# Optimization experiments

Measured on AMD Instinct MI355X. Metric: run time of the kernel, lower is better.

The kernel has to match this reference:

```python
import jax, jax.numpy as jnp
import numpy as np

N, K, C_S, C_Z, C_G, N_RBF = 1024, 16, 256, 128, 16, 64
EPS = 1e-8


def _ln(x, g, b, eps=1e-5):
    m = x.mean(-1, keepdims=True)
    v = jnp.mean((x - m) ** 2, -1, keepdims=True)
    return (x - m) * jax.lax.rsqrt(v + eps) * g + b


def _rbf(D, D_count=N_RBF, D_min=0.0, D_max=20.0):
    mu = jnp.linspace(D_min, D_max, D_count, dtype=D.dtype)
    sigma = (D_max - D_min) / D_count
    return jnp.exp(-(((D[..., None] - mu) / sigma) ** 2))


def setup_inputs() -> dict:
    key = jax.random.key(0)
    ks = jax.random.split(key, 20)
    node_features = jax.random.normal(ks[0], (N, C_S), jnp.float32)
    trans = jax.random.normal(ks[1], (N, 3), jnp.float32) * 5.0  # CA translations, Angstrom-ish
    edge_features = jax.random.normal(ks[2], (N * K, C_Z), jnp.float32)
    # sparse graph laid out as K neighbors per node: dst = node i repeated K times
    src = jax.random.randint(ks[3], (N * K,), 0, N)
    dst = jnp.repeat(jnp.arange(N), K)
    edge_index = jnp.stack([src, dst]).astype(jnp.int64)
    batch = jnp.zeros((N,), jnp.int64)
    res_mask = jnp.ones((N,), bool)
    w = lambda k, i, o: jax.random.normal(k, (i, o), jnp.float32) * 0.02
    return {
        "node_features": node_features, "trans": trans, "edge_features": edge_features,
        "ln_g": jnp.ones((C_Z,), jnp.float32), "ln_b": jnp.zeros((C_Z,), jnp.float32),
        "Wl": w(ks[4], C_S, C_G), "bl": jnp.zeros((C_G,), jnp.float32),
        "Wr": w(ks[5], C_S, C_G), "br": jnp.zeros((C_G,), jnp.float32),
        "Wep": w(ks[6], C_Z, C_Z), "bep": jnp.zeros((C_Z,), jnp.float32),
        "Weg": w(ks[7], C_Z, C_Z), "beg": jnp.zeros((C_Z,), jnp.float32),
        "Wdg": w(ks[8], C_G * C_G, C_Z), "bdg": jnp.zeros((C_Z,), jnp.float32),
        "Wdp": w(ks[9], N_RBF, C_Z), "bdp": jnp.zeros((C_Z,), jnp.float32),
        "lno_g": jnp.ones((C_Z,), jnp.float32), "lno_b": jnp.zeros((C_Z,), jnp.float32),
        "Wout": w(ks[10], C_Z, C_Z), "bout": jnp.zeros((C_Z,), jnp.float32),
        "Wog": w(ks[11], C_Z, C_Z), "bog": jnp.zeros((C_Z,), jnp.float32),
        "edge_index": edge_index, "batch": batch, "res_mask": res_mask,
    }


def reference(node_features, trans, edge_features, ln_g, ln_b, Wl, bl, Wr, br,
              Wep, bep, Weg, beg, Wdg, bdg, Wdp, bdp, lno_g, lno_b, Wout, bout,
              Wog, bog, edge_index, batch, res_mask):
    n = node_features.shape[0]
    src = edge_index[0].reshape(n, K)              # neighbor indices per node [N,K]
    # sparse -> kNN: edges are grouped K per destination node
    knn_feats = edge_features.reshape(n, K, C_Z)
    knn_mask = res_mask[src] & res_mask[:, None]   # [N,K]
    z = _ln(knn_feats, ln_g, ln_b)
    # outer-product node gating
    nl = node_features @ Wl + bl                   # [N,c_g]
    nr = node_features @ Wr + br
    a = nl[src]                                    # [N,K,c_g]
    b = nr[src]
    edge3 = a[:, :, None, :, None] * b[:, None, :, None, :]   # [N,K,K,c_g,c_g]
    gate3 = edge3.reshape(n, K, K, C_G * C_G) @ Wdg + bdg     # [N,K,K,c_z]
    # RBF distance features among the K neighbors of each node
    t = trans[src]                                 # [N,K,3]
    d = jnp.linalg.norm(t[:, :, None, :] - t[:, None, :, :] + EPS, axis=-1)  # [N,K,K]
    df = _rbf(d) @ Wdp + bdp                       # [N,K,K,c_z]
    m2 = (knn_mask[:, :, None] & knn_mask[:, None, :]).astype(df.dtype)
    e3 = jax.nn.sigmoid(gate3) * df * m2[..., None]
    # gated edge projection
    e2 = jax.nn.sigmoid(z @ Weg + beg) * (z @ Wep + bep)      # [N,K,c_z]
    # triangle matmul: per channel c, [K,K] @ [K]
    upd = jnp.einsum('njkc,nkc->njc', e3, e2)                 # [N,K,c_z]
    upd = _ln(upd, lno_g, lno_b) @ Wout + bout
    upd = upd * jax.nn.sigmoid(z @ Wog + bog)
    # kNN -> sparse scatter back (masked)
    out = (upd * knn_mask[..., None].astype(upd.dtype)).reshape(n * K, C_Z)
    return out
```

## Files before the change

kernel.cpp:

```cpp
#include <hip/hip_runtime.h>
#include <hip/hip_bf16.h>
#include <math.h>

#define KNN  16
#define CZ   128
#define CG   16
#define CS   256
#define NRBF 64
#define NN   1024

typedef __attribute__((ext_vector_type(8))) _Float16 half8;
typedef __attribute__((ext_vector_type(4))) _Float16 half4;
typedef __attribute__((ext_vector_type(2))) _Float16 half2v;
typedef __attribute__((ext_vector_type(4))) float f4_t;

#define MFMA16x32(A, B, C) __builtin_amdgcn_mfma_f32_16x16x32_f16((A), (B), (C), 0, 0, 0)
#define MFMA16x16(A, B, C) __builtin_amdgcn_mfma_f32_16x16x16f16((A), (B), (C), 0, 0, 0)

union U8 { half2v h[4]; half8 v; };
union U4 { half2v h[2]; half4 v; };

__device__ __forceinline__ half2v pk2(float x, float y) {
    auto t = __builtin_amdgcn_cvt_pkrtz(x, y);
    half2v r;
    __builtin_memcpy(&r, &t, 4);
    return r;
}
__device__ __forceinline__ float sig_(float x) {
    return __builtin_amdgcn_rcpf(1.0f + __expf(-x));
}

__global__ __launch_bounds__(256) void prep_kernel(
    const float* __restrict__ Wdp, const float* __restrict__ Wdg,
    const float* __restrict__ Wout, const float* __restrict__ Wep,
    const float* __restrict__ Weg, const float* __restrict__ Wog,
    _Float16* __restrict__ pk,
    const float* __restrict__ nf,
    const float* __restrict__ Wl, const float* __restrict__ bl,
    const float* __restrict__ Wr, const float* __restrict__ br,
    float* __restrict__ nlo, float* __restrict__ nro) {
    int b = blockIdx.x, tid = threadIdx.x;
    if (b < 416) {
        int gid = b * 256 + tid;
        float val;
        if (gid >= 8192 && gid < 40960) {
            int o = gid - 8192;
            int i = o & 3, l = (o >> 2) & 63, ct = (o >> 8) & 7, q = o >> 11;
            int row = (4 * (l >> 4) + i) * 16 + q;
            int col = ct * 16 + (l & 15);
            val = Wdg[row * CZ + col];
        } else {
            const float* srcw;
            int o;
            if (gid < 8192)        { srcw = Wdp;  o = gid; }
            else if (gid < 57344)  { srcw = Wout; o = gid - 40960; }
            else if (gid < 73728)  { srcw = Wep;  o = gid - 57344; }
            else if (gid < 90112)  { srcw = Weg;  o = gid - 73728; }
            else                   { srcw = Wog;  o = gid - 90112; }
            int t = o & 7, l = (o >> 3) & 63, ct = (o >> 9) & 7, s = o >> 12;
            int row = s * 32 + (l >> 4) * 8 + t;
            int col = ct * 16 + (l & 15);
            val = srcw[row * CZ + col];
        }
        pk[gid] = (_Float16)val;
    } else {
        int grp = tid >> 6, lane = tid & 63;
        int n = (b - 416) * 4 + grp;
        int p = lane & 15, seg = lane >> 4;
        float accl = (seg == 0) ? bl[p] : 0.0f;
        float accr = (seg == 0) ? br[p] : 0.0f;
        const float* rw = nf + n * CS + seg * 64;
        for (int i = 0; i < 64; ++i) {
            float v = rw[i];
            int s = seg * 64 + i;
            accl += v * Wl[s * CG + p];
            accr += v * Wr[s * CG + p];
        }
        accl += __shfl_xor(accl, 16); accl += __shfl_xor(accl, 32);
        accr += __shfl_xor(accr, 16); accr += __shfl_xor(accr, 32);
        if (lane < 16) { nlo[n * CG + lane] = accl; nro[n * CG + lane] = accr; }
    }
}

__global__ __launch_bounds__(256) void main_kernel(
    const float* __restrict__ trans, const float* __restrict__ ef,
    const float* __restrict__ lng, const float* __restrict__ lnb,
    const float* __restrict__ nl, const float* __restrict__ nr,
    const float* __restrict__ bep, const float* __restrict__ beg,
    const float* __restrict__ bog,
    const _Float16* __restrict__ Wepp, const _Float16* __restrict__ Wegp,
    const _Float16* __restrict__ Wogp,
    const _Float16* __restrict__ Wdg2, const float* __restrict__ bdg,
    const _Float16* __restrict__ Wdpp, const float* __restrict__ bdp,
    const float* __restrict__ lnog, const float* __restrict__ lnob,
    const _Float16* __restrict__ Woutp, const float* __restrict__ bout,
    const int* __restrict__ src, const int* __restrict__ resmask,
    float* __restrict__ out) {
    __shared__ _Float16 s_z[16 * 136];
    __shared__ float s_t[16 * 4];
    __shared__ float s_km[16];
    __shared__ int   s_src[16];
    __shared__ float s_a[16 * 16];
    __shared__ float s_b[16 * 20];
    __shared__ _Float16 s_T[4][8192];
    __shared__ _Float16 s_upd[16 * 136];

    int n = blockIdx.x, tid = threadIdx.x;
    if (tid < 16) {
        int sv = src[n * KNN + tid];
        s_src[tid] = sv;
        s_km[tid] = (resmask[sv] != 0 && resmask[n] != 0) ? 1.0f : 0.0f;
        s_t[tid * 4 + 0] = trans[sv * 3 + 0];
        s_t[tid * 4 + 1] = trans[sv * 3 + 1];
        s_t[tid * 4 + 2] = trans[sv * 3 + 2];
    }
    __syncthreads();
    {
        int j = tid >> 4, p = tid & 15;
        int sv = s_src[j];
        s_a[j * 16 + p] = nl[sv * CG + p];
        s_b[j * 20 + p] = nr[sv * CG + p];
    }
    {
        int r = tid >> 4, seg = tid & 15;
        const float* row = ef + ((size_t)n * KNN + r) * CZ + seg * 8;
        f4_t x0 = *(const f4_t*)row;
        f4_t x1 = *(const f4_t*)(row + 4);
        float s = x0.x + x0.y + x0.z + x0.w + x1.x + x1.y + x1.z + x1.w;
        float q = x0.x * x0.x + x0.y * x0.y + x0.z * x0.z + x0.w * x0.w
                + x1.x * x1.x + x1.y * x1.y + x1.z * x1.z + x1.w * x1.w;
        #pragma unroll
        for (int m = 1; m < 16; m <<= 1) { s += __shfl_xor(s, m); q += __shfl_xor(q, m); }
        float mean = s * (1.0f / CZ);
        float var  = q * (1.0f / CZ) - mean * mean;
        float rs   = __builtin_amdgcn_rsqf(var + 1e-5f);
        int col = seg * 8;
        f4_t g0 = *(const f4_t*)(lng + col), g1 = *(const f4_t*)(lng + col + 4);
        f4_t b0 = *(const f4_t*)(lnb + col), b1 = *(const f4_t*)(lnb + col + 4);
        U8 zu;
        zu.h[0] = pk2((x0.x - mean) * rs * g0.x + b0.x, (x0.y - mean) * rs * g0.y + b0.y);
        zu.h[1] = pk2((x0.z - mean) * rs * g0.z + b0.z, (x0.w - mean) * rs * g0.w + b0.w);
        zu.h[2] = pk2((x1.x - mean) * rs * g1.x + b1.x, (x1.y - mean) * rs * g1.y + b1.y);
        zu.h[3] = pk2((x1.z - mean) * rs * g1.z + b1.z, (x1.w - mean) * rs * g1.w + b1.w);
        *(half8*)&s_z[r * 136 + col] = zu.v;
    }
    __syncthreads();

    int wv = tid >> 6, lane = tid & 63, l15 = lane & 15, quad = lane >> 4;

    half8 Az[4];
    #pragma unroll
    for (int st = 0; st < 4; ++st)
        Az[st] = *(const half8*)&s_z[l15 * 136 + st * 32 + quad * 8];
    f4_t e2f[2], ggf[2];
    #pragma unroll
    for (int cc = 0; cc < 2; ++cc) {
        int ct = wv * 2 + cc;
        int c = ct * 16 + l15;
        float vep = bep[c], veg = beg[c], vog = bog[c];
        f4_t aep = {vep, vep, vep, vep};
        f4_t aeg = {veg, veg, veg, veg};
        f4_t aog = {vog, vog, vog, vog};
        #pragma unroll
        for (int st = 0; st < 4; ++st) {
            int off = ((st * 8 + ct) * 64 + lane) * 8;
            half8 wep_ = *(const half8*)(Wepp + off);
            half8 weg_ = *(const half8*)(Wegp + off);
            half8 wog_ = *(const half8*)(Wogp + off);
            aep = MFMA16x32(Az[st], wep_, aep);
            aeg = MFMA16x32(Az[st], weg_, aeg);
            aog = MFMA16x32(Az[st], wog_, aog);
        }
        #pragma unroll
        for (int rr = 0; rr < 4; ++rr) {
            e2f[cc][rr] = sig_(aeg[rr]) * aep[rr] * s_km[quad * 4 + rr];
            ggf[cc][rr] = sig_(aog[rr]);
        }
    }

    half8 Bdp[2][2];
    #pragma unroll
    for (int st = 0; st < 2; ++st)
        #pragma unroll
        for (int cc = 0; cc < 2; ++cc)
            Bdp[st][cc] = *(const half8*)(Wdpp + ((st * 8 + wv * 2 + cc) * 64 + lane) * 8);

    half4 Aa, Ab;
    {
        f4_t av = *(const f4_t*)&s_a[l15 * 16 + 4 * quad];
        U4 u; u.h[0] = pk2(av.x, av.y); u.h[1] = pk2(av.z, av.w);
        Aa = u.v;
        f4_t bv = *(const f4_t*)&s_b[l15 * 20 + 4 * quad];
        U4 w; w.h[0] = pk2(bv.x, bv.y); w.h[1] = pk2(bv.z, bv.w);
        Ab = w.v;
    }
    _Float16* Tw = s_T[wv];
    #pragma unroll
    for (int ctl = 0; ctl < 2; ++ctl) {
        int ct = wv * 2 + ctl;
        #pragma unroll
        for (int q0 = 0; q0 < 16; q0 += 4) {
            f4_t tq[4];
            #pragma unroll
            for (int qq = 0; qq < 4; ++qq) {
                half4 Bw = *(const half4*)(Wdg2 + (((q0 + qq) * 8 + ct) * 64 + lane) * 4);
                f4_t z = {0.f, 0.f, 0.f, 0.f};
                tq[qq] = MFMA16x16(Aa, Bw, z);
            }
            #pragma unroll
            for (int rr = 0; rr < 4; ++rr) {
                U4 u;
                u.h[0] = pk2(tq[0][rr], tq[1][rr]);
                u.h[1] = pk2(tq[2][rr], tq[3][rr]);
                *(half4*)&Tw[(((4 * quad + rr) * 2 + ctl) * 16 + l15) * 16 + q0] = u.v;
            }
        }
    }

    float bdgv[2], bdpv[2];
    #pragma unroll
    for (int cc = 0; cc < 2; ++cc) {
        int c = (wv * 2 + cc) * 16 + l15;
        bdgv[cc] = bdg[c];
        bdpv[cc] = bdp[c];
    }
    float tkx = s_t[l15 * 4 + 0], tky = s_t[l15 * 4 + 1], tkz = s_t[l15 * 4 + 2];
    const float MUS = 20.0f / 63.0f;
    const float ISG = 1.0f / 0.3125f;
    float rIS[2];
    #pragma unroll
    for (int st = 0; st < 2; ++st)
        rIS[st] = (float)(st * 32 + quad * 8) * (MUS * ISG);

    for (int j = 0; j < 16; ++j) {
        float dx = s_t[j * 4 + 0] - tkx + 1e-8f;
        float dy = s_t[j * 4 + 1] - tky + 1e-8f;
        float dz = s_t[j * 4 + 2] - tkz + 1e-8f;
        float dI = sqrtf(dx * dx + dy * dy + dz * dz) * ISG;

        half8 ar[2];
        #pragma unroll
        for (int st = 0; st < 2; ++st) {
            U8 cv;
            float base0 = dI - rIS[st];
            #pragma unroll
            for (int tt = 0; tt < 4; ++tt) {
                float u0 = base0 - (float)(2 * tt) * (MUS * ISG);
                float u1 = u0 - (MUS * ISG);
                cv.h[tt] = pk2(__expf(-u0 * u0), __expf(-u1 * u1));
            }
            ar[st] = cv.v;
        }
        f4_t accd[2], accg[2];
        #pragma unroll
        for (int cc = 0; cc < 2; ++cc) {
            f4_t z = {bdpv[cc], bdpv[cc], bdpv[cc], bdpv[cc]};
            z = MFMA16x32(ar[0], Bdp[0][cc], z);
            z = MFMA16x32(ar[1], Bdp[1][cc], z);
            accd[cc] = z;
            half4 Bt = *(const half4*)&Tw[((j * 2 + cc) * 16 + l15) * 16 + 4 * quad];
            f4_t g = {bdgv[cc], bdgv[cc], bdgv[cc], bdgv[cc]};
            accg[cc] = MFMA16x16(Ab, Bt, g);
        }
        float kmj = s_km[j];
        #pragma unroll
        for (int cc = 0; cc < 2; ++cc) {
            float part = 0.f;
            #pragma unroll
            for (int rr = 0; rr < 4; ++rr)
                part += sig_(accg[cc][rr]) * accd[cc][rr] * e2f[cc][rr];
            part += __shfl_xor(part, 16);
            part += __shfl_xor(part, 32);
            if (lane < 16)
                s_upd[j * 136 + (wv * 2 + cc) * 16 + lane] = (_Float16)(part * kmj);
        }
    }
    __syncthreads();

    #pragma unroll
    for (int rr2 = 0; rr2 < 4; ++rr2) {
        int rj = wv * 4 + rr2;
        float x0 = (float)s_upd[rj * 136 + lane];
        float x1 = (float)s_upd[rj * 136 + 64 + lane];
        float sm = x0 + x1, sq = x0 * x0 + x1 * x1;
        #pragma unroll
        for (int m = 1; m < 64; m <<= 1) {
            sm += __shfl_xor(sm, m);
            sq += __shfl_xor(sq, m);
        }
        float mean = sm * (1.0f / CZ);
        float var  = sq * (1.0f / CZ) - mean * mean;
        float rsv  = __builtin_amdgcn_rsqf(var + 1e-5f);
        float h0 = (x0 - mean) * rsv * lnog[lane] + lnob[lane];
        float h1 = (x1 - mean) * rsv * lnog[64 + lane] + lnob[64 + lane];
        s_z[rj * 136 + lane]      = (_Float16)h0;
        s_z[rj * 136 + 64 + lane] = (_Float16)h1;
    }
    __syncthreads();

    half8 Aw[4];
    #pragma unroll
    for (int st = 0; st < 4; ++st)
        Aw[st] = *(const half8*)&s_z[l15 * 136 + st * 32 + quad * 8];
    #pragma unroll
    for (int cc = 0; cc < 2; ++cc) {
        int c = (wv * 2 + cc) * 16 + l15;
        float bo = bout[c];
        f4_t acc = {bo, bo, bo, bo};
        #pragma unroll
        for (int st = 0; st < 4; ++st) {
            half8 bw = *(const half8*)(Woutp + ((st * 8 + wv * 2 + cc) * 64 + lane) * 8);
            acc = MFMA16x32(Aw[st], bw, acc);
        }
        #pragma unroll
        for (int rr = 0; rr < 4; ++rr) {
            int row = quad * 4 + rr;
            size_t oi = (size_t)(n * KNN + row) * CZ + c;
            out[oi] = acc[rr] * ggf[cc][rr] * s_km[row];
        }
    }
}

extern "C" void kernel_launch(void* const* d_in, const int* in_sizes, int n_in,
                              void* d_out, int out_size, void* d_ws, size_t ws_size,
                              hipStream_t stream) {
    const float* node_features = (const float*)d_in[0];
    const float* trans         = (const float*)d_in[1];
    const float* edge_features = (const float*)d_in[2];
    const float* ln_g  = (const float*)d_in[3];
    const float* ln_b  = (const float*)d_in[4];
    const float* Wl    = (const float*)d_in[5];
    const float* bl    = (const float*)d_in[6];
    const float* Wr    = (const float*)d_in[7];
    const float* br    = (const float*)d_in[8];
    const float* Wep   = (const float*)d_in[9];
    const float* bep   = (const float*)d_in[10];
    const float* Weg   = (const float*)d_in[11];
    const float* beg   = (const float*)d_in[12];
    const float* Wdg   = (const float*)d_in[13];
    const float* bdg   = (const float*)d_in[14];
    const float* Wdp   = (const float*)d_in[15];
    const float* bdp   = (const float*)d_in[16];
    const float* lno_g = (const float*)d_in[17];
    const float* lno_b = (const float*)d_in[18];
    const float* Wout  = (const float*)d_in[19];
    const float* bout  = (const float*)d_in[20];
    const float* Wog   = (const float*)d_in[21];
    const float* bog   = (const float*)d_in[22];
    const int* edge_index = (const int*)d_in[23];
    const int* resmask    = (const int*)d_in[25];

    float* ws = (float*)d_ws;
    float* nl = ws;
    float* nr = nl + NN * CG;
    _Float16* pk = (_Float16*)(nr + NN * CG);
    _Float16* Wdpp  = pk;
    _Float16* Wdg2  = pk + 8192;
    _Float16* Woutp = pk + 40960;
    _Float16* Wepp  = pk + 57344;
    _Float16* Wegp  = pk + 73728;
    _Float16* Wogp  = pk + 90112;
    const int* src = edge_index;

    prep_kernel<<<672, 256, 0, stream>>>(
        Wdp, Wdg, Wout, Wep, Weg, Wog, pk,
        node_features, Wl, bl, Wr, br, nl, nr);
    main_kernel<<<NN, 256, 0, stream>>>(
        trans, edge_features, ln_g, ln_b, nl, nr,
        bep, beg, bog, Wepp, Wegp, Wogp,
        Wdg2, bdg, Wdpp, bdp, lno_g, lno_b,
        Woutp, bout, src, resmask, (float*)d_out);
}
```

Before: 163.2 us.

## Fuse weight prep and node projections into single kernel, halve triangle LDS buffer

Removes the separate prep kernel that repacked weights to fp16 and computed per-node left/right projections. The main kernel now reads fp32 weights directly with strided gathers and converts them into MFMA fragments in registers, and it computes the neighbor projections with MFMA per block. The Wdg-derived T buffer is built in two halves of eight neighbors each, shrinking LDS so more blocks can be resident. The cost is redundant uncoalesced weight loads and conversions in every block, plus recomputing T twice per half.

```diff
diff --git a/kernel.cpp b/kernel.cpp
--- a/kernel.cpp
+++ b/kernel.cpp
@@ -1,12 +1,10 @@
 #include <hip/hip_runtime.h>
-#include <hip/hip_bf16.h>
 #include <math.h>
 
 #define KNN  16
 #define CZ   128
 #define CG   16
 #define CS   256
-#define NRBF 64
 #define NN   1024
 
 typedef __attribute__((ext_vector_type(8))) _Float16 half8;
@@ -30,79 +28,53 @@
     return __builtin_amdgcn_rcpf(1.0f + __expf(-x));
 }
 
-__global__ __launch_bounds__(256) void prep_kernel(
-    const float* __restrict__ Wdp, const float* __restrict__ Wdg,
-    const float* __restrict__ Wout, const float* __restrict__ Wep,
-    const float* __restrict__ Weg, const float* __restrict__ Wog,
-    _Float16* __restrict__ pk,
-    const float* __restrict__ nf,
+__device__ __forceinline__ half8 gfrag(const float* __restrict__ W,
+                                       int st, int ct, int lane) {
+    int row = st * 32 + ((lane >> 4) << 3);
+    int col = ct * 16 + (lane & 15);
+    const float* p = W + row * CZ + col;
+    float v0 = p[0 * CZ], v1 = p[1 * CZ], v2 = p[2 * CZ], v3 = p[3 * CZ];
+    float v4 = p[4 * CZ], v5 = p[5 * CZ], v6 = p[6 * CZ], v7 = p[7 * CZ];
+    U8 u;
+    u.h[0] = pk2(v0, v1); u.h[1] = pk2(v2, v3);
+    u.h[2] = pk2(v4, v5); u.h[3] = pk2(v6, v7);
+    return u.v;
+}
+
+__device__ __forceinline__ half4 gfrag16(const float* __restrict__ Wdg,
+                                         int q, int ct, int lane) {
+    int quad = lane >> 4;
+    int col = ct * 16 + (lane & 15);
+    const float* p = Wdg + (4 * quad * 16 + q) * CZ + col;
+    float v0 = p[0 * 16 * CZ], v1 = p[1 * 16 * CZ];
+    float v2 = p[2 * 16 * CZ], v3 = p[3 * 16 * CZ];
+    U4 u;
+    u.h[0] = pk2(v0, v1); u.h[1] = pk2(v2, v3);
+    return u.v;
+}
+
+__global__ __launch_bounds__(256) void fused_kernel(
+    const float* __restrict__ nf, const float* __restrict__ trans,
+    const float* __restrict__ ef,
+    const float* __restrict__ lng, const float* __restrict__ lnb,
     const float* __restrict__ Wl, const float* __restrict__ bl,
     const float* __restrict__ Wr, const float* __restrict__ br,
-    float* __restrict__ nlo, float* __restrict__ nro) {
-    int b = blockIdx.x, tid = threadIdx.x;
-    if (b < 416) {
-        int gid = b * 256 + tid;
-        float val;
-        if (gid >= 8192 && gid < 40960) {
-            int o = gid - 8192;
-            int i = o & 3, l = (o >> 2) & 63, ct = (o >> 8) & 7, q = o >> 11;
-            int row = (4 * (l >> 4) + i) * 16 + q;
-            int col = ct * 16 + (l & 15);
-            val = Wdg[row * CZ + col];
-        } else {
-            const float* srcw;
-            int o;
-            if (gid < 8192)        { srcw = Wdp;  o = gid; }
-            else if (gid < 57344)  { srcw = Wout; o = gid - 40960; }
-            else if (gid < 73728)  { srcw = Wep;  o = gid - 57344; }
-            else if (gid < 90112)  { srcw = Weg;  o = gid - 73728; }
-            else                   { srcw = Wog;  o = gid - 90112; }
-            int t = o & 7, l = (o >> 3) & 63, ct = (o >> 9) & 7, s = o >> 12;
-            int row = s * 32 + (l >> 4) * 8 + t;
-            int col = ct * 16 + (l & 15);
-            val = srcw[row * CZ + col];
-        }
-        pk[gid] = (_Float16)val;
-    } else {
-        int grp = tid >> 6, lane = tid & 63;
-        int n = (b - 416) * 4 + grp;
-        int p = lane & 15, seg = lane >> 4;
-        float accl = (seg == 0) ? bl[p] : 0.0f;
-        float accr = (seg == 0) ? br[p] : 0.0f;
-        const float* rw = nf + n * CS + seg * 64;
-        for (int i = 0; i < 64; ++i) {
-            float v = rw[i];
-            int s = seg * 64 + i;
-            accl += v * Wl[s * CG + p];
-            accr += v * Wr[s * CG + p];
-        }
-        accl += __shfl_xor(accl, 16); accl += __shfl_xor(accl, 32);
-        accr += __shfl_xor(accr, 16); accr += __shfl_xor(accr, 32);
-        if (lane < 16) { nlo[n * CG + lane] = accl; nro[n * CG + lane] = accr; }
-    }
-}
-
-__global__ __launch_bounds__(256) void main_kernel(
-    const float* __restrict__ trans, const float* __restrict__ ef,
-    const float* __restrict__ lng, const float* __restrict__ lnb,
-    const float* __restrict__ nl, const float* __restrict__ nr,
-    const float* __restrict__ bep, const float* __restrict__ beg,
-    const float* __restrict__ bog,
-    const _Float16* __restrict__ Wepp, const _Float16* __restrict__ Wegp,
-    const _Float16* __restrict__ Wogp,
-    const _Float16* __restrict__ Wdg2, const float* __restrict__ bdg,
-    const _Float16* __restrict__ Wdpp, const float* __restrict__ bdp,
+    const float* __restrict__ Wep, const float* __restrict__ bep,
+    const float* __restrict__ Weg, const float* __restrict__ beg,
+    const float* __restrict__ Wdg, const float* __restrict__ bdg,
+    const float* __restrict__ Wdp, const float* __restrict__ bdp,
     const float* __restrict__ lnog, const float* __restrict__ lnob,
-    const _Float16* __restrict__ Woutp, const float* __restrict__ bout,
+    const float* __restrict__ Wout, const float* __restrict__ bout,
+    const float* __restrict__ Wog, const float* __restrict__ bog,
     const int* __restrict__ src, const int* __restrict__ resmask,
     float* __restrict__ out) {
     __shared__ _Float16 s_z[16 * 136];
-    __shared__ float s_t[16 * 4];
+    __shared__ float s_t[64];
     __shared__ float s_km[16];
     __shared__ int   s_src[16];
-    __shared__ float s_a[16 * 16];
+    __shared__ float s_a[256];
     __shared__ float s_b[16 * 20];
-    __shared__ _Float16 s_T[4][8192];
+    __shared__ _Float16 s_T[4 * 5120];
     __shared__ _Float16 s_upd[16 * 136];
 
     int n = blockIdx.x, tid = threadIdx.x;
@@ -115,12 +87,9 @@
         s_t[tid * 4 + 2] = trans[sv * 3 + 2];
     }
     __syncthreads();
-    {
-        int j = tid >> 4, p = tid & 15;
-        int sv = s_src[j];
-        s_a[j * 16 + p] = nl[sv * CG + p];
-        s_b[j * 20 + p] = nr[sv * CG + p];
-    }
+
+    int wv = tid >> 6, lane = tid & 63, l15 = lane & 15, quad = lane >> 4;
+
     {
         int r = tid >> 4, seg = tid & 15;
         const float* row = ef + ((size_t)n * KNN + r) * CZ + seg * 8;
@@ -144,9 +113,35 @@
         zu.h[3] = pk2((x1.z - mean) * rs * g1.z + b1.z, (x1.w - mean) * rs * g1.w + b1.w);
         *(half8*)&s_z[r * 136 + col] = zu.v;
     }
+
+    if (wv < 2) {
+        const float* W16 = wv ? Wr : Wl;
+        const float* bb  = wv ? br : bl;
+        const float* arow = nf + (size_t)s_src[l15] * CS;
+        float bv = bb[l15];
+        f4_t acc = {bv, bv, bv, bv};
+        #pragma unroll
+        for (int st = 0; st < 8; ++st) {
+            f4_t x0 = *(const f4_t*)(arow + st * 32 + quad * 8);
+            f4_t x1 = *(const f4_t*)(arow + st * 32 + quad * 8 + 4);
+            U8 ua;
+            ua.h[0] = pk2(x0.x, x0.y); ua.h[1] = pk2(x0.z, x0.w);
+            ua.h[2] = pk2(x1.x, x1.y); ua.h[3] = pk2(x1.z, x1.w);
+            const float* wp = W16 + (st * 32 + quad * 8) * CG + l15;
+            float w0 = wp[0 * CG], w1 = wp[1 * CG], w2 = wp[2 * CG], w3 = wp[3 * CG];
+            float w4 = wp[4 * CG], w5 = wp[5 * CG], w6 = wp[6 * CG], w7 = wp[7 * CG];
+            U8 ub;
+            ub.h[0] = pk2(w0, w1); ub.h[1] = pk2(w2, w3);
+            ub.h[2] = pk2(w4, w5); ub.h[3] = pk2(w6, w7);
+            acc = MFMA16x32(ua.v, ub.v, acc);
+        }
+        float* dst = wv ? s_b : s_a;
+        int stride = wv ? 20 : 16;
+        #pragma unroll
+        for (int rr = 0; rr < 4; ++rr)
+            dst[(4 * quad + rr) * stride + l15] = acc[rr];
+    }
     __syncthreads();
-
-    int wv = tid >> 6, lane = tid & 63, l15 = lane & 15, quad = lane >> 4;
 
     half8 Az[4];
     #pragma unroll
@@ -163,13 +158,9 @@
         f4_t aog = {vog, vog, vog, vog};
         #pragma unroll
         for (int st = 0; st < 4; ++st) {
-            int off = ((st * 8 + ct) * 64 + lane) * 8;
-            half8 wep_ = *(const half8*)(Wepp + off);
-            half8 weg_ = *(const half8*)(Wegp + off);
-            half8 wog_ = *(const half8*)(Wogp + off);
-            aep = MFMA16x32(Az[st], wep_, aep);
-            aeg = MFMA16x32(Az[st], weg_, aeg);
-            aog = MFMA16x32(Az[st], wog_, aog);
+            aep = MFMA16x32(Az[st], gfrag(Wep, st, ct, lane), aep);
+            aeg = MFMA16x32(Az[st], gfrag(Weg, st, ct, lane), aeg);
+            aog = MFMA16x32(Az[st], gfrag(Wog, st, ct, lane), aog);
         }
         #pragma unroll
         for (int rr = 0; rr < 4; ++rr) {
@@ -178,12 +169,20 @@
         }
     }
 
-    half8 Bdp[2][2];
+    half8 Bdp_[2][2];
     #pragma unroll
     for (int st = 0; st < 2; ++st)
         #pragma unroll
         for (int cc = 0; cc < 2; ++cc)
-            Bdp[st][cc] = *(const half8*)(Wdpp + ((st * 8 + wv * 2 + cc) * 64 + lane) * 8);
+            Bdp_[st][cc] = gfrag(Wdp, st, wv * 2 + cc, lane);
+
+    float bdgv[2], bdpv[2];
+    #pragma unroll
+    for (int cc = 0; cc < 2; ++cc) {
+        int c = (wv * 2 + cc) * 16 + l15;
+        bdgv[cc] = bdg[c];
+        bdpv[cc] = bdp[c];
+    }
 
     half4 Aa, Ab;
     {
@@ -194,36 +193,7 @@
         U4 w; w.h[0] = pk2(bv.x, bv.y); w.h[1] = pk2(bv.z, bv.w);
         Ab = w.v;
     }
-    _Float16* Tw = s_T[wv];
-    #pragma unroll
-    for (int ctl = 0; ctl < 2; ++ctl) {
-        int ct = wv * 2 + ctl;
-        #pragma unroll
-        for (int q0 = 0; q0 < 16; q0 += 4) {
-            f4_t tq[4];
-            #pragma unroll
-            for (int qq = 0; qq < 4; ++qq) {
-                half4 Bw = *(const half4*)(Wdg2 + (((q0 + qq) * 8 + ct) * 64 + lane) * 4);
-                f4_t z = {0.f, 0.f, 0.f, 0.f};
-                tq[qq] = MFMA16x16(Aa, Bw, z);
-            }
-            #pragma unroll
-            for (int rr = 0; rr < 4; ++rr) {
-                U4 u;
-                u.h[0] = pk2(tq[0][rr], tq[1][rr]);
-                u.h[1] = pk2(tq[2][rr], tq[3][rr]);
-                *(half4*)&Tw[(((4 * quad + rr) * 2 + ctl) * 16 + l15) * 16 + q0] = u.v;
-            }
-        }
-    }
-
-    float bdgv[2], bdpv[2];
-    #pragma unroll
-    for (int cc = 0; cc < 2; ++cc) {
-        int c = (wv * 2 + cc) * 16 + l15;
-        bdgv[cc] = bdg[c];
-        bdpv[cc] = bdp[c];
-    }
+
     float tkx = s_t[l15 * 4 + 0], tky = s_t[l15 * 4 + 1], tkz = s_t[l15 * 4 + 2];
     const float MUS = 20.0f / 63.0f;
     const float ISG = 1.0f / 0.3125f;
@@ -232,47 +202,77 @@
     for (int st = 0; st < 2; ++st)
         rIS[st] = (float)(st * 32 + quad * 8) * (MUS * ISG);
 
-    for (int j = 0; j < 16; ++j) {
-        float dx = s_t[j * 4 + 0] - tkx + 1e-8f;
-        float dy = s_t[j * 4 + 1] - tky + 1e-8f;
-        float dz = s_t[j * 4 + 2] - tkz + 1e-8f;
-        float dI = sqrtf(dx * dx + dy * dy + dz * dz) * ISG;
-
-        half8 ar[2];
-        #pragma unroll
-        for (int st = 0; st < 2; ++st) {
-            U8 cv;
-            float base0 = dI - rIS[st];
+    _Float16* Tw = s_T + wv * 5120;
+    int jl_base = 4 * (quad & 1);
+    bool act_h[2] = {(quad >> 1) == 0, (quad >> 1) == 1};
+
+    for (int h = 0; h < 2; ++h) {
+        #pragma unroll
+        for (int ctl = 0; ctl < 2; ++ctl) {
+            int ct = wv * 2 + ctl;
             #pragma unroll
-            for (int tt = 0; tt < 4; ++tt) {
-                float u0 = base0 - (float)(2 * tt) * (MUS * ISG);
-                float u1 = u0 - (MUS * ISG);
-                cv.h[tt] = pk2(__expf(-u0 * u0), __expf(-u1 * u1));
+            for (int qb = 0; qb < 4; ++qb) {
+                f4_t tq[4];
+                #pragma unroll
+                for (int qq = 0; qq < 4; ++qq) {
+                    f4_t z = {0.f, 0.f, 0.f, 0.f};
+                    tq[qq] = MFMA16x16(Aa, gfrag16(Wdg, 4 * qb + qq, ct, lane), z);
+                }
+                if (act_h[h]) {
+                    #pragma unroll
+                    for (int rr = 0; rr < 4; ++rr) {
+                        U4 u;
+                        u.h[0] = pk2(tq[0][rr], tq[1][rr]);
+                        u.h[1] = pk2(tq[2][rr], tq[3][rr]);
+                        int jl = jl_base + rr;
+                        *(half4*)&Tw[(((jl * 2 + ctl) * 80) + l15 * 5 + qb) * 4] = u.v;
+                    }
+                }
             }
-            ar[st] = cv.v;
-        }
-        f4_t accd[2], accg[2];
-        #pragma unroll
-        for (int cc = 0; cc < 2; ++cc) {
-            f4_t z = {bdpv[cc], bdpv[cc], bdpv[cc], bdpv[cc]};
-            z = MFMA16x32(ar[0], Bdp[0][cc], z);
-            z = MFMA16x32(ar[1], Bdp[1][cc], z);
-            accd[cc] = z;
-            half4 Bt = *(const half4*)&Tw[((j * 2 + cc) * 16 + l15) * 16 + 4 * quad];
-            f4_t g = {bdgv[cc], bdgv[cc], bdgv[cc], bdgv[cc]};
-            accg[cc] = MFMA16x16(Ab, Bt, g);
-        }
-        float kmj = s_km[j];
-        #pragma unroll
-        for (int cc = 0; cc < 2; ++cc) {
-            float part = 0.f;
+        }
+
+        for (int j = 8 * h; j < 8 * h + 8; ++j) {
+            float dx = s_t[j * 4 + 0] - tkx + 1e-8f;
+            float dy = s_t[j * 4 + 1] - tky + 1e-8f;
+            float dz = s_t[j * 4 + 2] - tkz + 1e-8f;
+            float dI = sqrtf(dx * dx + dy * dy + dz * dz) * ISG;
+
+            half8 ar[2];
             #pragma unroll
-            for (int rr = 0; rr < 4; ++rr)
-                part += sig_(accg[cc][rr]) * accd[cc][rr] * e2f[cc][rr];
-            part += __shfl_xor(part, 16);
-            part += __shfl_xor(part, 32);
-            if (lane < 16)
-                s_upd[j * 136 + (wv * 2 + cc) * 16 + lane] = (_Float16)(part * kmj);
+            for (int st = 0; st < 2; ++st) {
+                U8 cv;
+                float base0 = dI - rIS[st];
+                #pragma unroll
+                for (int tt = 0; tt < 4; ++tt) {
+                    float u0 = base0 - (float)(2 * tt) * (MUS * ISG);
+                    float u1 = u0 - (MUS * ISG);
+                    cv.h[tt] = pk2(__expf(-u0 * u0), __expf(-u1 * u1));
+                }
+                ar[st] = cv.v;
+            }
+            f4_t accd[2], accg[2];
+            #pragma unroll
+            for (int cc = 0; cc < 2; ++cc) {
+                f4_t z = {bdpv[cc], bdpv[cc], bdpv[cc], bdpv[cc]};
+                z = MFMA16x32(ar[0], Bdp_[0][cc], z);
+                z = MFMA16x32(ar[1], Bdp_[1][cc], z);
+                accd[cc] = z;
+                half4 Bt = *(const half4*)&Tw[(((j & 7) * 2 + cc) * 80 + l15 * 5 + quad) * 4];
+                f4_t g = {bdgv[cc], bdgv[cc], bdgv[cc], bdgv[cc]};
+                accg[cc] = MFMA16x16(Ab, Bt, g);
+            }
+            float kmj = s_km[j];
+            #pragma unroll
+            for (int cc = 0; cc < 2; ++cc) {
+                float part = 0.f;
+                #pragma unroll
+                for (int rr = 0; rr < 4; ++rr)
+                    part += sig_(accg[cc][rr]) * accd[cc][rr] * e2f[cc][rr];
+                part += __shfl_xor(part, 16);
+                part += __shfl_xor(part, 32);
+                if (lane < 16)
+                    s_upd[j * 136 + (wv * 2 + cc) * 16 + lane] = (_Float16)(part * kmj);
+            }
         }
     }
     __syncthreads();
@@ -304,14 +304,13 @@
         Aw[st] = *(const half8*)&s_z[l15 * 136 + st * 32 + quad * 8];
     #pragma unroll
     for (int cc = 0; cc < 2; ++cc) {
-        int c = (wv * 2 + cc) * 16 + l15;
+        int ct = wv * 2 + cc;
+        int c = ct * 16 + l15;
         float bo = bout[c];
         f4_t acc = {bo, bo, bo, bo};
         #pragma unroll
-        for (int st = 0; st < 4; ++st) {
-            half8 bw = *(const half8*)(Woutp + ((st * 8 + wv * 2 + cc) * 64 + lane) * 8);
-            acc = MFMA16x32(Aw[st], bw, acc);
-        }
+        for (int st = 0; st < 4; ++st)
+            acc = MFMA16x32(Aw[st], gfrag(Wout, st, ct, lane), acc);
         #pragma unroll
         for (int rr = 0; rr < 4; ++rr) {
             int row = quad * 4 + rr;
@@ -349,25 +348,10 @@
     const float* bog   = (const float*)d_in[22];
     const int* edge_index = (const int*)d_in[23];
     const int* resmask    = (const int*)d_in[25];
-
-    float* ws = (float*)d_ws;
-    float* nl = ws;
-    float* nr = nl + NN * CG;
-    _Float16* pk = (_Float16*)(nr + NN * CG);
-    _Float16* Wdpp  = pk;
-    _Float16* Wdg2  = pk + 8192;
-    _Float16* Woutp = pk + 40960;
-    _Float16* Wepp  = pk + 57344;
-    _Float16* Wegp  = pk + 73728;
-    _Float16* Wogp  = pk + 90112;
     const int* src = edge_index;
 
-    prep_kernel<<<672, 256, 0, stream>>>(
-        Wdp, Wdg, Wout, Wep, Weg, Wog, pk,
-        node_features, Wl, bl, Wr, br, nl, nr);
-    main_kernel<<<NN, 256, 0, stream>>>(
-        trans, edge_features, ln_g, ln_b, nl, nr,
-        bep, beg, bog, Wepp, Wegp, Wogp,
-        Wdg2, bdg, Wdpp, bdp, lno_g, lno_b,
-        Woutp, bout, src, resmask, (float*)d_out);
-}
+    fused_kernel<<<NN, 256, 0, stream>>>(
+        node_features, trans, edge_features, ln_g, ln_b,
+        Wl, bl, Wr, br, Wep, bep, Weg, beg, Wdg, bdg, Wdp, bdp,
+        lno_g, lno_b, Wout, bout, Wog, bog, src, resmask, (float*)d_out);
+}
```

Result: slower. 213.3 us (+30.7%).

## Stage Wdg projection in two halves with padded LDS to cut shared memory

Applied to the files above, without the earlier changes.

The per-wave staging buffer for the Wdg-projected edge features now covers only 8 neighbor rows at a time instead of all 16. The projection MFMAs are recomputed for each half, and only the quads owning that half write. Rows are padded to a stride of 5 half4 groups to avoid LDS bank conflicts. This shrinks shared memory per block so more blocks can reside per CU, at the cost of doubling the Wdg MFMA work.

```diff
diff --git a/kernel.cpp b/kernel.cpp
--- a/kernel.cpp
+++ b/kernel.cpp
@@ -1,12 +1,10 @@
 #include <hip/hip_runtime.h>
-#include <hip/hip_bf16.h>
 #include <math.h>
 
 #define KNN  16
 #define CZ   128
 #define CG   16
 #define CS   256
-#define NRBF 64
 #define NN   1024
 
 typedef __attribute__((ext_vector_type(8))) _Float16 half8;
@@ -97,12 +95,12 @@
     const int* __restrict__ src, const int* __restrict__ resmask,
     float* __restrict__ out) {
     __shared__ _Float16 s_z[16 * 136];
-    __shared__ float s_t[16 * 4];
+    __shared__ float s_t[64];
     __shared__ float s_km[16];
     __shared__ int   s_src[16];
-    __shared__ float s_a[16 * 16];
+    __shared__ float s_a[256];
     __shared__ float s_b[16 * 20];
-    __shared__ _Float16 s_T[4][8192];
+    __shared__ _Float16 s_T[4 * 5120];
     __shared__ _Float16 s_upd[16 * 136];
 
     int n = blockIdx.x, tid = threadIdx.x;
@@ -178,12 +176,20 @@
         }
     }
 
-    half8 Bdp[2][2];
+    half8 Bdp_[2][2];
     #pragma unroll
     for (int st = 0; st < 2; ++st)
         #pragma unroll
         for (int cc = 0; cc < 2; ++cc)
-            Bdp[st][cc] = *(const half8*)(Wdpp + ((st * 8 + wv * 2 + cc) * 64 + lane) * 8);
+            Bdp_[st][cc] = *(const half8*)(Wdpp + ((st * 8 + wv * 2 + cc) * 64 + lane) * 8);
+
+    float bdgv[2], bdpv[2];
+    #pragma unroll
+    for (int cc = 0; cc < 2; ++cc) {
+        int c = (wv * 2 + cc) * 16 + l15;
+        bdgv[cc] = bdg[c];
+        bdpv[cc] = bdp[c];
+    }
 
     half4 Aa, Ab;
     {
@@ -194,36 +200,7 @@
         U4 w; w.h[0] = pk2(bv.x, bv.y); w.h[1] = pk2(bv.z, bv.w);
         Ab = w.v;
     }
-    _Float16* Tw = s_T[wv];
-    #pragma unroll
-    for (int ctl = 0; ctl < 2; ++ctl) {
-        int ct = wv * 2 + ctl;
-        #pragma unroll
-        for (int q0 = 0; q0 < 16; q0 += 4) {
-            f4_t tq[4];
-            #pragma unroll
-            for (int qq = 0; qq < 4; ++qq) {
-                half4 Bw = *(const half4*)(Wdg2 + (((q0 + qq) * 8 + ct) * 64 + lane) * 4);
-                f4_t z = {0.f, 0.f, 0.f, 0.f};
-                tq[qq] = MFMA16x16(Aa, Bw, z);
-            }
-            #pragma unroll
-            for (int rr = 0; rr < 4; ++rr) {
-                U4 u;
-                u.h[0] = pk2(tq[0][rr], tq[1][rr]);
-                u.h[1] = pk2(tq[2][rr], tq[3][rr]);
-                *(half4*)&Tw[(((4 * quad + rr) * 2 + ctl) * 16 + l15) * 16 + q0] = u.v;
-            }
-        }
-    }
-
-    float bdgv[2], bdpv[2];
-    #pragma unroll
-    for (int cc = 0; cc < 2; ++cc) {
-        int c = (wv * 2 + cc) * 16 + l15;
-        bdgv[cc] = bdg[c];
-        bdpv[cc] = bdp[c];
-    }
+
     float tkx = s_t[l15 * 4 + 0], tky = s_t[l15 * 4 + 1], tkz = s_t[l15 * 4 + 2];
     const float MUS = 20.0f / 63.0f;
     const float ISG = 1.0f / 0.3125f;
@@ -232,47 +209,78 @@
     for (int st = 0; st < 2; ++st)
         rIS[st] = (float)(st * 32 + quad * 8) * (MUS * ISG);
 
-    for (int j = 0; j < 16; ++j) {
-        float dx = s_t[j * 4 + 0] - tkx + 1e-8f;
-        float dy = s_t[j * 4 + 1] - tky + 1e-8f;
-        float dz = s_t[j * 4 + 2] - tkz + 1e-8f;
-        float dI = sqrtf(dx * dx + dy * dy + dz * dz) * ISG;
-
-        half8 ar[2];
-        #pragma unroll
-        for (int st = 0; st < 2; ++st) {
-            U8 cv;
-            float base0 = dI - rIS[st];
+    _Float16* Tw = s_T + wv * 5120;
+    int jl_base = 4 * (quad & 1);
+    int myh = quad >> 1;
+
+    for (int h = 0; h < 2; ++h) {
+        #pragma unroll
+        for (int ctl = 0; ctl < 2; ++ctl) {
+            int ct = wv * 2 + ctl;
             #pragma unroll
-            for (int tt = 0; tt < 4; ++tt) {
-                float u0 = base0 - (float)(2 * tt) * (MUS * ISG);
-                float u1 = u0 - (MUS * ISG);
-                cv.h[tt] = pk2(__expf(-u0 * u0), __expf(-u1 * u1));
+            for (int qb = 0; qb < 4; ++qb) {
+                f4_t tq[4];
+                #pragma unroll
+                for (int qq = 0; qq < 4; ++qq) {
+                    half4 Bw = *(const half4*)(Wdg2 + (((4 * qb + qq) * 8 + ct) * 64 + lane) * 4);
+                    f4_t z = {0.f, 0.f, 0.f, 0.f};
+                    tq[qq] = MFMA16x16(Aa, Bw, z);
+                }
+                if (myh == h) {
+                    #pragma unroll
+                    for (int rr = 0; rr < 4; ++rr) {
+                        U4 u;
+                        u.h[0] = pk2(tq[0][rr], tq[1][rr]);
+                        u.h[1] = pk2(tq[2][rr], tq[3][rr]);
+                        int jl = jl_base + rr;
+                        *(half4*)&Tw[(((jl * 2 + ctl) * 80) + l15 * 5 + qb) * 4] = u.v;
+                    }
+                }
             }
-            ar[st] = cv.v;
-        }
-        f4_t accd[2], accg[2];
-        #pragma unroll
-        for (int cc = 0; cc < 2; ++cc) {
-            f4_t z = {bdpv[cc], bdpv[cc], bdpv[cc], bdpv[cc]};
-            z = MFMA16x32(ar[0], Bdp[0][cc], z);
-            z = MFMA16x32(ar[1], Bdp[1][cc], z);
-            accd[cc] = z;
-            half4 Bt = *(const half4*)&Tw[((j * 2 + cc) * 16 + l15) * 16 + 4 * quad];
-            f4_t g = {bdgv[cc], bdgv[cc], bdgv[cc], bdgv[cc]};
-            accg[cc] = MFMA16x16(Ab, Bt, g);
-        }
-        float kmj = s_km[j];
-        #pragma unroll
-        for (int cc = 0; cc < 2; ++cc) {
-            float part = 0.f;
+        }
+
+        for (int j = 8 * h; j < 8 * h + 8; ++j) {
+            float dx = s_t[j * 4 + 0] - tkx + 1e-8f;
+            float dy = s_t[j * 4 + 1] - tky + 1e-8f;
+            float dz = s_t[j * 4 + 2] - tkz + 1e-8f;
+            float dI = sqrtf(dx * dx + dy * dy + dz * dz) * ISG;
+
+            half8 ar[2];
             #pragma unroll
-            for (int rr = 0; rr < 4; ++rr)
-                part += sig_(accg[cc][rr]) * accd[cc][rr] * e2f[cc][rr];
-            part += __shfl_xor(part, 16);
-            part += __shfl_xor(part, 32);
-            if (lane < 16)
-                s_upd[j * 136 + (wv * 2 + cc) * 16 + lane] = (_Float16)(part * kmj);
+            for (int st = 0; st < 2; ++st) {
+                U8 cv;
+                float base0 = dI - rIS[st];
+                #pragma unroll
+                for (int tt = 0; tt < 4; ++tt) {
+                    float u0 = base0 - (float)(2 * tt) * (MUS * ISG);
+                    float u1 = u0 - (MUS * ISG);
+                    cv.h[tt] = pk2(__expf(-u0 * u0), __expf(-u1 * u1));
+                }
+                ar[st] = cv.v;
+            }
+            f4_t accd[2], accg[2];
+            #pragma unroll
+            for (int cc = 0; cc < 2; ++cc) {
+                f4_t z = {bdpv[cc], bdpv[cc], bdpv[cc], bdpv[cc]};
+                z = MFMA16x32(ar[0], Bdp_[0][cc], z);
+                z = MFMA16x32(ar[1], Bdp_[1][cc], z);
+                accd[cc] = z;
+                half4 Bt = *(const half4*)&Tw[(((j & 7) * 2 + cc) * 80 + l15 * 5 + quad) * 4];
+                f4_t g = {bdgv[cc], bdgv[cc], bdgv[cc], bdgv[cc]};
+                accg[cc] = MFMA16x16(Ab, Bt, g);
+            }
+            float kmj = s_km[j];
+            #pragma unroll
+            for (int cc = 0; cc < 2; ++cc) {
+                float part = 0.f;
+                #pragma unroll
+                for (int rr = 0; rr < 4; ++rr)
+                    part += sig_(accg[cc][rr]) * accd[cc][rr] * e2f[cc][rr];
+                part += __shfl_xor(part, 16);
+                part += __shfl_xor(part, 32);
+                if (lane < 16)
+                    s_upd[j * 136 + (wv * 2 + cc) * 16 + lane] = (_Float16)(part * kmj);
+            }
         }
     }
     __syncthreads();
@@ -304,12 +312,13 @@
         Aw[st] = *(const half8*)&s_z[l15 * 136 + st * 32 + quad * 8];
     #pragma unroll
     for (int cc = 0; cc < 2; ++cc) {
-        int c = (wv * 2 + cc) * 16 + l15;
+        int ct = wv * 2 + cc;
+        int c = ct * 16 + l15;
         float bo = bout[c];
         f4_t acc = {bo, bo, bo, bo};
         #pragma unroll
         for (int st = 0; st < 4; ++st) {
-            half8 bw = *(const half8*)(Woutp + ((st * 8 + wv * 2 + cc) * 64 + lane) * 8);
+            half8 bw = *(const half8*)(Woutp + ((st * 8 + ct) * 64 + lane) * 8);
             acc = MFMA16x32(Aw[st], bw, acc);
         }
         #pragma unroll
```

Measured after the change: 172.9 us. +6.0%, slower.
